# Optimization experiments

Measured on AMD Instinct MI355X. Metric: run time of the kernel, lower is better.

The kernel has to match this reference:

```python
import jax, jax.numpy as jnp
import numpy as np

N0, N1, N2 = 200000, 600000, 400000
NNZ1, NNZ2 = 1200000, 1200000
G = 256          # number of graphs in the batch
H = 128          # num_hidden
NIN = 32         # num_input
L = 2            # num_layers
R = 3            # max_rank + 1


def setup_inputs() -> dict:
    key = jax.random.key(0)
    ks = jax.random.split(key, 24)
    d = {}
    d["x0"] = jax.random.normal(ks[0], (N0, NIN), jnp.float32)
    d["x1"] = jax.random.normal(ks[1], (N1, NIN), jnp.float32)
    d["x2"] = jax.random.normal(ks[2], (N2, NIN), jnp.float32)
    d["b1_rows"] = jax.random.randint(ks[3], (NNZ1,), 0, N0, jnp.int32)
    d["b1_cols"] = jax.random.randint(ks[4], (NNZ1,), 0, N1, jnp.int32)
    d["b2_rows"] = jax.random.randint(ks[5], (NNZ2,), 0, N1, jnp.int32)
    d["b2_cols"] = jax.random.randint(ks[6], (NNZ2,), 0, N2, jnp.int32)
    d["batch0"] = jnp.sort(jax.random.randint(ks[7], (N0,), 0, G, jnp.int32))
    d["batch1"] = jnp.sort(jax.random.randint(ks[8], (N1,), 0, G, jnp.int32))
    d["batch2"] = jnp.sort(jax.random.randint(ks[9], (N2,), 0, G, jnp.int32))
    sin = 1.0 / np.sqrt(NIN).astype(np.float32)
    sh = 1.0 / np.sqrt(H).astype(np.float32)
    d["w_emb"] = jax.random.normal(ks[10], (NIN, H), jnp.float32) * sin
    d["b_emb"] = jnp.zeros((H,), jnp.float32)
    # one conv weight per (layer, rank>0): message W for B_r^T @ (x @ W)
    d["conv_w"] = jax.random.normal(ks[11], (L, 2, H, H), jnp.float32) * sh
    d["pre_w1"] = jax.random.normal(ks[12], (R, H, H), jnp.float32) * sh
    d["pre_b1"] = jnp.zeros((R, H), jnp.float32)
    d["pre_w2"] = jax.random.normal(ks[13], (R, H, H), jnp.float32) * sh
    d["pre_b2"] = jnp.zeros((R, H), jnp.float32)
    d["post_w1"] = jax.random.normal(ks[14], (R * H, H), jnp.float32) * (1.0 / np.sqrt(R * H).astype(np.float32))
    d["post_b1"] = jnp.zeros((H,), jnp.float32)
    d["post_w2"] = jax.random.normal(ks[15], (H, 1), jnp.float32) * sh
    d["post_b2"] = jnp.zeros((1,), jnp.float32)
    return d


def reference(x0, x1, x2, b1_rows, b1_cols, b2_rows, b2_cols,
              batch0, batch1, batch2,
              w_emb, b_emb, conv_w,
              pre_w1, pre_b1, pre_w2, pre_b2,
              post_w1, post_b1, post_w2, post_b2):
    # feature embedding (shared across ranks)
    h0 = x0 @ w_emb + b_emb
    h1 = x1 @ w_emb + b_emb
    h2 = x2 @ w_emb + b_emb

    for l in range(L):
        # sparse incidence matmul B_r^T @ h_{r-1}: gather rows, scatter-add to cols
        m1 = jax.ops.segment_sum(h0[b1_rows], b1_cols, num_segments=N1)
        m2 = jax.ops.segment_sum(h1[b2_rows], b2_cols, num_segments=N2)
        # aggregation with sigmoid update; rank 0 has no incoming messages
        h0 = jax.nn.sigmoid(h0)
        h1 = jax.nn.sigmoid(m1 @ conv_w[l, 0])
        h2 = jax.nn.sigmoid(m2 @ conv_w[l, 1])

    def pre_pool(h, r):
        z = jax.nn.silu(h @ pre_w1[r] + pre_b1[r])
        return z @ pre_w2[r] + pre_b2[r]

    # global_add_pool per rank -> [G, H] each
    p0 = jax.ops.segment_sum(pre_pool(h0, 0), batch0, num_segments=G)
    p1 = jax.ops.segment_sum(pre_pool(h1, 1), batch1, num_segments=G)
    p2 = jax.ops.segment_sum(pre_pool(h2, 2), batch2, num_segments=G)

    state = jnp.concatenate([p0, p1, p2], axis=1)  # [G, 3H]
    z = jax.nn.silu(state @ post_w1 + post_b1)
    out = z @ post_w2 + post_b2                     # [G, 1]
    return jnp.squeeze(out, axis=-1)                # [G]
```

## Files before the change

### kernel.cpp

```cpp
#include <hip/hip_runtime.h>
#include <math.h>

#define HDIM 128
#define NIN_ 32
#define RANKS 3

typedef unsigned int u32;
typedef unsigned short u16;
typedef __attribute__((ext_vector_type(8))) short short8;
typedef __attribute__((ext_vector_type(8))) __bf16 bf16x8;
typedef __attribute__((ext_vector_type(4))) float f32x4;

__device__ __forceinline__ float bf2f(u16 b) { return __uint_as_float(((u32)b) << 16); }
__device__ __forceinline__ u16 f2bf(float f) {
    u32 u = __float_as_uint(f);
    u32 r = u + 0x7fffu + ((u >> 16) & 1u);
    return (u16)(r >> 16);
}
__device__ __forceinline__ float sigmoidf_(float x) {
    return __builtin_amdgcn_rcpf(1.0f + __builtin_amdgcn_exp2f(-1.44269504f * x));
}
__device__ __forceinline__ float siluf_(float x) { return x * sigmoidf_(x); }

template <int SIG>
__device__ __forceinline__ float sigpow(float f) {
#pragma unroll
    for (int q = 0; q < SIG; ++q) f = sigmoidf_(f);
    return f;
}

__global__ void zero_kernel(u32* __restrict__ p, long long nw) {
    long long i = (long long)blockIdx.x * blockDim.x + threadIdx.x;
    long long stride = (long long)gridDim.x * blockDim.x;
    for (; i < nw; i += stride) p[i] = 0u;
}

__global__ void count_kernel(const int* __restrict__ cols, int* __restrict__ cnt, int nnz) {
    int e = blockIdx.x * 256 + threadIdx.x;
    if (e < nnz) atomicAdd(&cnt[cols[e]], 1);
}

__global__ void scan1_kernel(const int* __restrict__ cnt, int* __restrict__ bsum, int ndst) {
    __shared__ int lds[256];
    int base = blockIdx.x * 1024, t = threadIdx.x;
    int s = 0;
#pragma unroll
    for (int j = 0; j < 4; ++j) {
        int i = base + t * 4 + j;
        s += (i < ndst) ? cnt[i] : 0;
    }
    lds[t] = s;
    __syncthreads();
    for (int off = 128; off > 0; off >>= 1) {
        if (t < off) lds[t] += lds[t + off];
        __syncthreads();
    }
    if (t == 0) bsum[blockIdx.x] = lds[0];
}

__global__ void scan2_kernel(int* __restrict__ bsum, int nb, int* __restrict__ total) {
    __shared__ int lds[256];
    int t = threadIdx.x;
    int v[8];
    int s = 0;
#pragma unroll
    for (int j = 0; j < 8; ++j) {
        int i = t * 8 + j;
        v[j] = (i < nb) ? bsum[i] : 0;
        s += v[j];
    }
    lds[t] = s;
    __syncthreads();
    for (int off = 1; off < 256; off <<= 1) {
        int y = (t >= off) ? lds[t - off] : 0;
        __syncthreads();
        lds[t] += y;
        __syncthreads();
    }
    int run = lds[t] - s;
#pragma unroll
    for (int j = 0; j < 8; ++j) {
        int i = t * 8 + j;
        if (i < nb) {
            bsum[i] = run;
            run += v[j];
        }
    }
    if (t == 255) *total = run;
}

__global__ void scan3_kernel(const int* __restrict__ cnt, const int* __restrict__ bsum,
                             int* __restrict__ rowptr, int* __restrict__ cursor, int ndst) {
    __shared__ int lds[256];
    int base = blockIdx.x * 1024, t = threadIdx.x;
    int v[4];
    int s = 0;
#pragma unroll
    for (int j = 0; j < 4; ++j) {
        int i = base + t * 4 + j;
        v[j] = (i < ndst) ? cnt[i] : 0;
        s += v[j];
    }
    lds[t] = s;
    __syncthreads();
    for (int off = 1; off < 256; off <<= 1) {
        int y = (t >= off) ? lds[t - off] : 0;
        __syncthreads();
        lds[t] += y;
        __syncthreads();
    }
    int run = bsum[blockIdx.x] + lds[t] - s;
#pragma unroll
    for (int j = 0; j < 4; ++j) {
        int i = base + t * 4 + j;
        if (i < ndst) {
            rowptr[i] = run;
            cursor[i] = run;
            run += v[j];
        }
    }
}

__global__ void fill_kernel(const int* __restrict__ rows, const int* __restrict__ cols,
                            int* __restrict__ cursor, int* __restrict__ esrc, int nnz) {
    int e = blockIdx.x * 256 + threadIdx.x;
    if (e >= nnz) return;
    int idx = atomicAdd(&cursor[cols[e]], 1);
    esrc[idx] = rows[e];
}

__global__ void wprep_kernel(const float* __restrict__ conv_w, const float* __restrict__ pre_w1,
                             const float* __restrict__ pre_w2, u16* __restrict__ wt, int Lnum) {
    int tid = blockIdx.x * 256 + threadIdx.x;
    int nm = 2 * Lnum + 6;
    if (tid >= nm * 128 * 128) return;
    int m = tid >> 14;
    int r = tid & 16383;
    int k = r >> 7;
    int col = r & 127;
    const float* src;
    if (m < 2 * Lnum) src = conv_w + (size_t)m * 16384;
    else if (m < 2 * Lnum + 3) src = pre_w1 + (size_t)(m - 2 * Lnum) * 16384;
    else src = pre_w2 + (size_t)(m - 2 * Lnum - 3) * 16384;
    float v = src[k * 128 + col];
    wt[(size_t)m * 16384 + col * 128 + (k ^ ((col & 7) << 3))] = f2bf(v);
}

__global__ void wembprep_kernel(const float* __restrict__ w_emb, u16* __restrict__ wembT) {
    int tid = blockIdx.x * 256 + threadIdx.x;
    if (tid >= HDIM * NIN_) return;
    int col = tid >> 5, k = tid & 31;
    wembT[col * 32 + k] = f2bf(w_emb[k * HDIM + col]);
}

__global__ __launch_bounds__(512) void embed_mfma_kernel(const float* __restrict__ x,
                                                         const u16* __restrict__ wembT,
                                                         const float* __restrict__ b,
                                                         u16* __restrict__ h, int n) {
    __shared__ u16 cs[8][16][128];
    const int tid = threadIdx.x;
    const int wave = tid >> 6, lane = tid & 63;
    const int row0 = blockIdx.x * 128;
    const int col = lane & 15, kg = lane >> 4;
    const int wrow0 = row0 + wave * 16;
    const int arow = wrow0 + col;
    const int arowc = arow < n ? arow : (n - 1);

    bf16x8 afrag;
    {
        const float4* xp = (const float4*)(x + (size_t)arowc * NIN_ + kg * 8);
        float4 xa = xp[0], xb = xp[1];
        short8 s;
        s[0] = (short)f2bf(xa.x); s[1] = (short)f2bf(xa.y);
        s[2] = (short)f2bf(xa.z); s[3] = (short)f2bf(xa.w);
        s[4] = (short)f2bf(xb.x); s[5] = (short)f2bf(xb.y);
        s[6] = (short)f2bf(xb.z); s[7] = (short)f2bf(xb.w);
        afrag = __builtin_bit_cast(bf16x8, s);
    }

#pragma unroll
    for (int ct = 0; ct < 8; ++ct) {
        int bcol = ct * 16 + col;
        bf16x8 bfrag = *(const bf16x8*)(wembT + bcol * 32 + kg * 8);
        f32x4 acc = (f32x4){0.f, 0.f, 0.f, 0.f};
        acc = __builtin_amdgcn_mfma_f32_16x16x32_bf16(afrag, bfrag, acc, 0, 0, 0);
        float bv = b[bcol];
#pragma unroll
        for (int r = 0; r < 4; ++r) {
            int crow = kg * 4 + r;
            cs[wave][crow][(ct * 16 + col) ^ ((crow & 7) << 3)] = f2bf(acc[r] + bv);
        }
    }
#pragma unroll
    for (int it = 0; it < 4; ++it) {
        int cid = it * 64 + lane;
        int r = cid >> 4, c = cid & 15;
        int grow = wrow0 + r;
        if (grow < n) {
            short8 v = *(const short8*)(&cs[wave][r][(c * 8) ^ ((r & 7) << 3)]);
            *(short8*)(h + (size_t)grow * HDIM + c * 8) = v;
        }
    }
}

__device__ __forceinline__ void gemm128(const bf16x8 afrag[4], const u16* wls, f32x4 acc[8],
                                        int col, int kg) {
#pragma unroll
    for (int ct = 0; ct < 8; ++ct) {
        int bcol = ct * 16 + col;
        const u16* bb = wls + bcol * 128;
        int swz = (bcol & 7) << 3;
#pragma unroll
        for (int k0 = 0; k0 < 4; ++k0) {
            bf16x8 bfrag = *(const bf16x8*)(bb + ((k0 * 32 + kg * 8) ^ swz));
            acc[ct] = __builtin_amdgcn_mfma_f32_16x16x32_bf16(afrag[k0], bfrag, acc[ct], 0, 0, 0);
        }
    }
}

__device__ __forceinline__ void stage_w(const u16* __restrict__ w, u16* wls, int tid) {
    const uint4* g = (const uint4*)w;
    uint4* l = (uint4*)wls;
    for (int i = tid; i < 2048; i += 512) l[i] = g[i];
}

__device__ __forceinline__ void pool_acc(const f32x4 acc[8], const float* __restrict__ b2,
                                         const int* __restrict__ batch, float* __restrict__ p,
                                         int n, int colOff, int wrow0, int col, int kg) {
    if (wrow0 >= n) return;
    int rend = wrow0 + 15 < n ? wrow0 + 15 : (n - 1);
    int bstart = batch[wrow0];
    int bend = batch[rend];
    if (bstart == bend) {
#pragma unroll
        for (int ct = 0; ct < 8; ++ct) {
            float b2v = b2[ct * 16 + col];
            float s = 0.f;
#pragma unroll
            for (int r = 0; r < 4; ++r) {
                int row = wrow0 + kg * 4 + r;
                if (row < n) s += acc[ct][r] + b2v;
            }
            s += __shfl_xor(s, 16, 64);
            s += __shfl_xor(s, 32, 64);
            if (kg == 0) atomicAdd(&p[bstart * (RANKS * HDIM) + colOff + ct * 16 + col], s);
        }
    } else {
        int bgs[4];
#pragma unroll
        for (int r = 0; r < 4; ++r) {
            int row = wrow0 + kg * 4 + r;
            bgs[r] = (row < n) ? batch[row] : -1;
        }
#pragma unroll
        for (int ct = 0; ct < 8; ++ct) {
            float b2v = b2[ct * 16 + col];
            int curb = -1;
            float cur = 0.f;
#pragma unroll
            for (int r = 0; r < 4; ++r) {
                if (bgs[r] >= 0) {
                    if (bgs[r] != curb) {
                        if (curb >= 0)
                            atomicAdd(&p[curb * (RANKS * HDIM) + colOff + ct * 16 + col], cur);
                        curb = bgs[r];
                        cur = 0.f;
                    }
                    cur += acc[ct][r] + b2v;
                }
            }
            if (curb >= 0) atomicAdd(&p[curb * (RANKS * HDIM) + colOff + ct * 16 + col], cur);
        }
    }
}

template <int SIGA>
__global__ __launch_bounds__(512) void merged_n1_kernel(
    const u16* __restrict__ srcbuf, const int* __restrict__ rowptr,
    const int* __restrict__ esrc, const u16* __restrict__ wc0, const u16* __restrict__ wc1,
    const u16* __restrict__ w1t, const u16* __restrict__ w2t,
    const float* __restrict__ b1, const float* __restrict__ b2,
    const int* __restrict__ batch, float* __restrict__ p, int colOff,
    u16* __restrict__ outB, int n) {
    __shared__ u16 wls[16384];
    __shared__ u16 zs[8][16][128];
    const int tid = threadIdx.x;
    const int wave = tid >> 6, lane = tid & 63;
    const int row0 = blockIdx.x * 128;
    const int col = lane & 15, kg = lane >> 4;
    const int wrow0 = row0 + wave * 16;

    stage_w(wc0, wls, tid);

    float gr[4][8], gs[4][8];
#pragma unroll
    for (int k0 = 0; k0 < 4; ++k0)
#pragma unroll
        for (int j = 0; j < 8; ++j) { gr[k0][j] = 0.f; gs[k0][j] = 0.f; }

    const int arow = wrow0 + col;
    if (arow < n) {
        int beg = rowptr[arow], end = rowptr[arow + 1];
        for (int e = beg; e < end; e += 2) {
            int s0 = esrc[e];
            bool has1 = (e + 1 < end);
            int s1 = has1 ? esrc[e + 1] : s0;
            const bf16x8* p0 = (const bf16x8*)(srcbuf + (size_t)s0 * HDIM + kg * 8);
            const bf16x8* p1 = (const bf16x8*)(srcbuf + (size_t)s1 * HDIM + kg * 8);
            bf16x8 v0[4], v1[4];
#pragma unroll
            for (int k0 = 0; k0 < 4; ++k0) { v0[k0] = p0[k0 * 4]; v1[k0] = p1[k0 * 4]; }
#pragma unroll
            for (int k0 = 0; k0 < 4; ++k0) {
                short8 sv = __builtin_bit_cast(short8, v0[k0]);
#pragma unroll
                for (int j = 0; j < 8; ++j) {
                    float f = sigpow<SIGA>(bf2f((u16)sv[j]));
                    gr[k0][j] += f;
                    gs[k0][j] += sigmoidf_(f);
                }
            }
            if (has1) {
#pragma unroll
                for (int k0 = 0; k0 < 4; ++k0) {
                    short8 sv = __builtin_bit_cast(short8, v1[k0]);
#pragma unroll
                    for (int j = 0; j < 8; ++j) {
                        float f = sigpow<SIGA>(bf2f((u16)sv[j]));
                        gr[k0][j] += f;
                        gs[k0][j] += sigmoidf_(f);
                    }
                }
            }
        }
    }
    bf16x8 afragR[4], afragS[4];
#pragma unroll
    for (int k0 = 0; k0 < 4; ++k0) {
        short8 sR, sS;
#pragma unroll
        for (int j = 0; j < 8; ++j) {
            sR[j] = (short)f2bf(gr[k0][j]);
            sS[j] = (short)f2bf(gs[k0][j]);
        }
        afragR[k0] = __builtin_bit_cast(bf16x8, sR);
        afragS[k0] = __builtin_bit_cast(bf16x8, sS);
    }
    __syncthreads();

    f32x4 acc[8];
#pragma unroll
    for (int ct = 0; ct < 8; ++ct) acc[ct] = (f32x4){0.f, 0.f, 0.f, 0.f};
    gemm128(afragR, wls, acc, col, kg);
#pragma unroll
    for (int ct = 0; ct < 8; ++ct)
#pragma unroll
        for (int r = 0; r < 4; ++r) {
            int crow = kg * 4 + r;
            zs[wave][crow][(ct * 16 + col) ^ ((crow & 7) << 3)] = f2bf(sigmoidf_(acc[ct][r]));
        }
#pragma unroll
    for (int it = 0; it < 4; ++it) {
        int cid = it * 64 + lane;
        int r = cid >> 4, c = cid & 15;
        int grow = wrow0 + r;
        if (grow < n) {
            short8 v = *(const short8*)(&zs[wave][r][(c * 8) ^ ((r & 7) << 3)]);
            *(short8*)(outB + (size_t)grow * HDIM + c * 8) = v;
        }
    }

    __syncthreads();
    stage_w(wc1, wls, tid);
    __syncthreads();

#pragma unroll
    for (int ct = 0; ct < 8; ++ct) acc[ct] = (f32x4){0.f, 0.f, 0.f, 0.f};
    gemm128(afragS, wls, acc, col, kg);
#pragma unroll
    for (int ct = 0; ct < 8; ++ct)
#pragma unroll
        for (int r = 0; r < 4; ++r) {
            int crow = kg * 4 + r;
            zs[wave][crow][(ct * 16 + col) ^ ((crow & 7) << 3)] = f2bf(sigmoidf_(acc[ct][r]));
        }
    __syncthreads();
    stage_w(w1t, wls, tid);
    __syncthreads();

    bf16x8 zfrag[4];
    {
        int zswz = (col & 7) << 3;
#pragma unroll
        for (int k0 = 0; k0 < 4; ++k0)
            zfrag[k0] = *(const bf16x8*)(&zs[wave][col][(k0 * 32 + kg * 8) ^ zswz]);
    }
#pragma unroll
    for (int ct = 0; ct < 8; ++ct) acc[ct] = (f32x4){0.f, 0.f, 0.f, 0.f};
    gemm128(zfrag, wls, acc, col, kg);
#pragma unroll
    for (int ct = 0; ct < 8; ++ct) {
        float b1v = b1[ct * 16 + col];
#pragma unroll
        for (int r = 0; r < 4; ++r) {
            int crow = kg * 4 + r;
            zs[wave][crow][(ct * 16 + col) ^ ((crow & 7) << 3)] = f2bf(siluf_(acc[ct][r] + b1v));
        }
    }
    __syncthreads();
    stage_w(w2t, wls, tid);
    __syncthreads();

    {
        int zswz = (col & 7) << 3;
#pragma unroll
        for (int k0 = 0; k0 < 4; ++k0)
            zfrag[k0] = *(const bf16x8*)(&zs[wave][col][(k0 * 32 + kg * 8) ^ zswz]);
    }
#pragma unroll
    for (int ct = 0; ct < 8; ++ct) acc[ct] = (f32x4){0.f, 0.f, 0.f, 0.f};
    gemm128(zfrag, wls, acc, col, kg);

    pool_acc(acc, b2, batch, p, n, colOff, wrow0, col, kg);
}

template <int MODE, int SIG>
__global__ __launch_bounds__(512) void fused_mfma_kernel(
    const u16* __restrict__ srcbuf, const int* __restrict__ rowptr,
    const int* __restrict__ esrc, const u16* __restrict__ wconv,
    const u16* __restrict__ w1t, const u16* __restrict__ w2t,
    const float* __restrict__ b1, const float* __restrict__ b2,
    const int* __restrict__ batch, float* __restrict__ p, int colOff,
    u16* __restrict__ outB, int n) {
    __shared__ u16 wls[16384];
    __shared__ u16 zs[8][16][128];
    const int tid = threadIdx.x;
    const int wave = tid >> 6, lane = tid & 63;
    const int row0 = blockIdx.x * 128;
    const int col = lane & 15, kg = lane >> 4;
    const int wrow0 = row0 + wave * 16;

    stage_w(wconv, wls, tid);

    float ga[4][8];
#pragma unroll
    for (int k0 = 0; k0 < 4; ++k0)
#pragma unroll
        for (int j = 0; j < 8; ++j) ga[k0][j] = 0.f;
    const int arow = wrow0 + col;
    if (arow < n) {
        int beg = rowptr[arow], end = rowptr[arow + 1];
        for (int e = beg; e < end; e += 2) {
            int s0 = esrc[e];
            bool has1 = (e + 1 < end);
            int s1 = has1 ? esrc[e + 1] : s0;
            const bf16x8* p0 = (const bf16x8*)(srcbuf + (size_t)s0 * HDIM + kg * 8);
            const bf16x8* p1 = (const bf16x8*)(srcbuf + (size_t)s1 * HDIM + kg * 8);
            bf16x8 v0[4], v1[4];
#pragma unroll
            for (int k0 = 0; k0 < 4; ++k0) { v0[k0] = p0[k0 * 4]; v1[k0] = p1[k0 * 4]; }
#pragma unroll
            for (int k0 = 0; k0 < 4; ++k0) {
                short8 sv = __builtin_bit_cast(short8, v0[k0]);
#pragma unroll
                for (int j = 0; j < 8; ++j) ga[k0][j] += sigpow<SIG>(bf2f((u16)sv[j]));
            }
            if (has1) {
#pragma unroll
                for (int k0 = 0; k0 < 4; ++k0) {
                    short8 sv = __builtin_bit_cast(short8, v1[k0]);
#pragma unroll
                    for (int j = 0; j < 8; ++j) ga[k0][j] += sigpow<SIG>(bf2f((u16)sv[j]));
                }
            }
        }
    }
    bf16x8 afrag[4];
#pragma unroll
    for (int k0 = 0; k0 < 4; ++k0) {
        short8 s;
#pragma unroll
        for (int j = 0; j < 8; ++j) s[j] = (short)f2bf(ga[k0][j]);
        afrag[k0] = __builtin_bit_cast(bf16x8, s);
    }
    __syncthreads();

    f32x4 acc[8];
#pragma unroll
    for (int ct = 0; ct < 8; ++ct) acc[ct] = (f32x4){0.f, 0.f, 0.f, 0.f};
    gemm128(afrag, wls, acc, col, kg);

#pragma unroll
    for (int ct = 0; ct < 8; ++ct)
#pragma unroll
        for (int r = 0; r < 4; ++r) {
            int crow = kg * 4 + r;
            zs[wave][crow][(ct * 16 + col) ^ ((crow & 7) << 3)] = f2bf(sigmoidf_(acc[ct][r]));
        }

    if (MODE == 0) {
#pragma unroll
        for (int it = 0; it < 4; ++it) {
            int cid = it * 64 + lane;
            int r = cid >> 4, c = cid & 15;
            int grow = wrow0 + r;
            if (grow < n) {
                short8 v = *(const short8*)(&zs[wave][r][(c * 8) ^ ((r & 7) << 3)]);
                *(short8*)(outB + (size_t)grow * HDIM + c * 8) = v;
            }
        }
        return;
    }

    __syncthreads();
    stage_w(w1t, wls, tid);
    __syncthreads();

    bf16x8 zfrag[4];
    {
        int zswz = (col & 7) << 3;
#pragma unroll
        for (int k0 = 0; k0 < 4; ++k0)
            zfrag[k0] = *(const bf16x8*)(&zs[wave][col][(k0 * 32 + kg * 8) ^ zswz]);
    }
#pragma unroll
    for (int ct = 0; ct < 8; ++ct) acc[ct] = (f32x4){0.f, 0.f, 0.f, 0.f};
    gemm128(zfrag, wls, acc, col, kg);
#pragma unroll
    for (int ct = 0; ct < 8; ++ct) {
        float b1v = b1[ct * 16 + col];
#pragma unroll
        for (int r = 0; r < 4; ++r) {
            int crow = kg * 4 + r;
            zs[wave][crow][(ct * 16 + col) ^ ((crow & 7) << 3)] = f2bf(siluf_(acc[ct][r] + b1v));
        }
    }
    __syncthreads();
    stage_w(w2t, wls, tid);
    __syncthreads();

    {
        int zswz = (col & 7) << 3;
#pragma unroll
        for (int k0 = 0; k0 < 4; ++k0)
            zfrag[k0] = *(const bf16x8*)(&zs[wave][col][(k0 * 32 + kg * 8) ^ zswz]);
    }
#pragma unroll
    for (int ct = 0; ct < 8; ++ct) acc[ct] = (f32x4){0.f, 0.f, 0.f, 0.f};
    gemm128(zfrag, wls, acc, col, kg);

    pool_acc(acc, b2, batch, p, n, colOff, wrow0, col, kg);
}

template <int SIG>
__global__ __launch_bounds__(512) void prepool_mfma_kernel(
    const u16* __restrict__ h, const u16* __restrict__ w1t, const u16* __restrict__ w2t,
    const float* __restrict__ b1, const float* __restrict__ b2, const int* __restrict__ batch,
    float* __restrict__ p, int n, int colOff) {
    __shared__ u16 wls[16384];
    __shared__ u16 zs[8][16][128];
    const int tid = threadIdx.x;
    const int wave = tid >> 6, lane = tid & 63;
    const int row0 = blockIdx.x * 128;
    const int col = lane & 15, kg = lane >> 4;
    const int wrow0 = row0 + wave * 16;

    stage_w(w1t, wls, tid);

    const int arow = wrow0 + col;
    const int arowc = arow < n ? arow : (n - 1);
    bf16x8 afrag[4];
    {
        const bf16x8* ap = (const bf16x8*)(h + (size_t)arowc * HDIM + kg * 8);
#pragma unroll
        for (int k0 = 0; k0 < 4; ++k0) afrag[k0] = ap[k0 * 4];
    }
    if (SIG > 0) {
#pragma unroll
        for (int k0 = 0; k0 < 4; ++k0) {
            short8 s = __builtin_bit_cast(short8, afrag[k0]);
#pragma unroll
            for (int j = 0; j < 8; ++j) s[j] = (short)f2bf(sigpow<SIG>(bf2f((u16)s[j])));
            afrag[k0] = __builtin_bit_cast(bf16x8, s);
        }
    }
    __syncthreads();

    f32x4 acc[8];
#pragma unroll
    for (int ct = 0; ct < 8; ++ct) acc[ct] = (f32x4){0.f, 0.f, 0.f, 0.f};
    gemm128(afrag, wls, acc, col, kg);
#pragma unroll
    for (int ct = 0; ct < 8; ++ct) {
        float b1v = b1[ct * 16 + col];
#pragma unroll
        for (int r = 0; r < 4; ++r) {
            int crow = kg * 4 + r;
            zs[wave][crow][(ct * 16 + col) ^ ((crow & 7) << 3)] = f2bf(siluf_(acc[ct][r] + b1v));
        }
    }
    __syncthreads();
    stage_w(w2t, wls, tid);
    __syncthreads();

    bf16x8 zfrag[4];
    {
        int zswz = (col & 7) << 3;
#pragma unroll
        for (int k0 = 0; k0 < 4; ++k0)
            zfrag[k0] = *(const bf16x8*)(&zs[wave][col][(k0 * 32 + kg * 8) ^ zswz]);
    }
#pragma unroll
    for (int ct = 0; ct < 8; ++ct) acc[ct] = (f32x4){0.f, 0.f, 0.f, 0.f};
    gemm128(zfrag, wls, acc, col, kg);

    pool_acc(acc, b2, batch, p, n, colOff, wrow0, col, kg);
}

__global__ void final_kernel(const float* __restrict__ p, const float* __restrict__ w1,
                             const float* __restrict__ b1, const float* __restrict__ w2,
                             const float* __restrict__ b2, float* __restrict__ out) {
    const int g = blockIdx.x;
    const int c = threadIdx.x;
    const float* pg = p + g * (RANKS * HDIM);
    float acc = b1[c];
    for (int k = 0; k < RANKS * HDIM; ++k) acc = fmaf(pg[k], w1[k * HDIM + c], acc);
    float z = siluf_(acc);
    float v = z * w2[c];
#pragma unroll
    for (int off = 32; off > 0; off >>= 1) v += __shfl_down(v, off, 64);
    __shared__ float red[2];
    if ((c & 63) == 0) red[c >> 6] = v;
    __syncthreads();
    if (c == 0) out[g] = red[0] + red[1] + b2[0];
}

extern "C" void kernel_launch(void* const* d_in, const int* in_sizes, int n_in,
                              void* d_out, int out_size, void* d_ws, size_t ws_size,
                              hipStream_t stream) {
    const float* x0 = (const float*)d_in[0];
    const float* x1 = (const float*)d_in[1];
    const int* b1_rows = (const int*)d_in[3];
    const int* b1_cols = (const int*)d_in[4];
    const int* b2_rows = (const int*)d_in[5];
    const int* b2_cols = (const int*)d_in[6];
    const int* batch0 = (const int*)d_in[7];
    const int* batch1 = (const int*)d_in[8];
    const int* batch2 = (const int*)d_in[9];
    const float* w_emb = (const float*)d_in[10];
    const float* b_emb = (const float*)d_in[11];
    const float* conv_w = (const float*)d_in[12];
    const float* pre_w1 = (const float*)d_in[13];
    const float* pre_b1 = (const float*)d_in[14];
    const float* pre_w2 = (const float*)d_in[15];
    const float* pre_b2 = (const float*)d_in[16];
    const float* post_w1 = (const float*)d_in[17];
    const float* post_b1 = (const float*)d_in[18];
    const float* post_w2 = (const float*)d_in[19];
    const float* post_b2 = (const float*)d_in[20];

    const int N0 = in_sizes[0] / NIN_;
    const int N1 = in_sizes[1] / NIN_;
    const int N2 = in_sizes[2] / NIN_;
    const int NNZ1 = in_sizes[3];
    const int NNZ2 = in_sizes[5];
    const int L = in_sizes[12] / (2 * HDIM * HDIM);
    const int Gn = out_size;

    u16* A = (u16*)d_ws;
    u16* B = A + (size_t)N0 * HDIM;
    float* p = (float*)(B + (size_t)N1 * HDIM);
    u16* wt = (u16*)(p + (size_t)Gn * RANKS * HDIM);
    const u16* wt_conv = wt;
    const u16* wt_p1 = wt + (size_t)2 * L * 16384;
    const u16* wt_p2 = wt_p1 + (size_t)3 * 16384;
    u16* wembT = wt + (size_t)(2 * L + 6) * 16384;
    int* ip = (int*)(wembT + 4096);
    int* rowptr1 = ip;  ip += N1 + 1;
    int* rowptr2 = ip;  ip += N2 + 1;
    int* esrc1 = ip;    ip += NNZ1;
    int* esrc2 = ip;    ip += NNZ2;
    int maxN = N1 > N2 ? N1 : N2;
    int* cnt = ip;      ip += maxN;
    int* cursor = ip;   ip += maxN;
    int* bsum = ip;     ip += 2048;

    {
        int tot = (2 * L + 6) * 16384;
        wprep_kernel<<<(tot + 255) / 256, 256, 0, stream>>>(conv_w, pre_w1, pre_w2, wt, L);
        wembprep_kernel<<<16, 256, 0, stream>>>(w_emb, wembT);

        zero_kernel<<<512, 256, 0, stream>>>((u32*)cnt, N1);
        count_kernel<<<(NNZ1 + 255) / 256, 256, 0, stream>>>(b1_cols, cnt, NNZ1);
        int nb1 = (N1 + 1023) / 1024;
        scan1_kernel<<<nb1, 256, 0, stream>>>(cnt, bsum, N1);
        scan2_kernel<<<1, 256, 0, stream>>>(bsum, nb1, rowptr1 + N1);
        scan3_kernel<<<nb1, 256, 0, stream>>>(cnt, bsum, rowptr1, cursor, N1);
        fill_kernel<<<(NNZ1 + 255) / 256, 256, 0, stream>>>(b1_rows, b1_cols, cursor, esrc1, NNZ1);

        zero_kernel<<<512, 256, 0, stream>>>((u32*)cnt, N2);
        count_kernel<<<(NNZ2 + 255) / 256, 256, 0, stream>>>(b2_cols, cnt, NNZ2);
        int nb2 = (N2 + 1023) / 1024;
        scan1_kernel<<<nb2, 256, 0, stream>>>(cnt, bsum, N2);
        scan2_kernel<<<1, 256, 0, stream>>>(bsum, nb2, rowptr2 + N2);
        scan3_kernel<<<nb2, 256, 0, stream>>>(cnt, bsum, rowptr2, cursor, N2);
        fill_kernel<<<(NNZ2 + 255) / 256, 256, 0, stream>>>(b2_rows, b2_cols, cursor, esrc2, NNZ2);
    }

    embed_mfma_kernel<<<(N0 + 127) / 128, 512, 0, stream>>>(x0, wembT, b_emb, A, N0);

    zero_kernel<<<64, 256, 0, stream>>>((u32*)p, (long long)Gn * RANKS * HDIM);

    if (L >= 2) {
        int grid = (N1 + 127) / 128;
        const u16* wc0 = wt_conv + (size_t)((L - 2) * 2 + 0) * 16384;
        const u16* wc1 = wt_conv + (size_t)((L - 1) * 2 + 0) * 16384;
        switch (L - 2) {
            case 0: merged_n1_kernel<0><<<grid, 512, 0, stream>>>(
                        A, rowptr1, esrc1, wc0, wc1, wt_p1 + 16384, wt_p2 + 16384,
                        pre_b1 + HDIM, pre_b2 + HDIM, batch1, p, HDIM, B, N1); break;
            case 1: merged_n1_kernel<1><<<grid, 512, 0, stream>>>(
                        A, rowptr1, esrc1, wc0, wc1, wt_p1 + 16384, wt_p2 + 16384,
                        pre_b1 + HDIM, pre_b2 + HDIM, batch1, p, HDIM, B, N1); break;
            default: merged_n1_kernel<2><<<grid, 512, 0, stream>>>(
                        A, rowptr1, esrc1, wc0, wc1, wt_p1 + 16384, wt_p2 + 16384,
                        pre_b1 + HDIM, pre_b2 + HDIM, batch1, p, HDIM, B, N1); break;
        }
    } else {
        embed_mfma_kernel<<<(N1 + 127) / 128, 512, 0, stream>>>(x1, wembT, b_emb, B, N1);
        fused_mfma_kernel<1, 0><<<(N1 + 127) / 128, 512, 0, stream>>>(
            A, rowptr1, esrc1, wt_conv, wt_p1 + 16384, wt_p2 + 16384,
            pre_b1 + HDIM, pre_b2 + HDIM, batch1, p, HDIM, nullptr, N1);
    }

    fused_mfma_kernel<1, 0><<<(N2 + 127) / 128, 512, 0, stream>>>(
        B, rowptr2, esrc2, wt_conv + (size_t)((L - 1) * 2 + 1) * 16384,
        wt_p1 + 2 * 16384, wt_p2 + 2 * 16384, pre_b1 + 2 * HDIM, pre_b2 + 2 * HDIM,
        batch2, p, 2 * HDIM, nullptr, N2);

    {
        int grid = (N0 + 127) / 128;
        switch (L) {
            case 1: prepool_mfma_kernel<1><<<grid, 512, 0, stream>>>(
                        A, wt_p1, wt_p2, pre_b1, pre_b2, batch0, p, N0, 0); break;
            case 2: prepool_mfma_kernel<2><<<grid, 512, 0, stream>>>(
                        A, wt_p1, wt_p2, pre_b1, pre_b2, batch0, p, N0, 0); break;
            default: prepool_mfma_kernel<3><<<grid, 512, 0, stream>>>(
                        A, wt_p1, wt_p2, pre_b1, pre_b2, batch0, p, N0, 0); break;
        }
    }

    final_kernel<<<Gn, HDIM, 0, stream>>>(p, post_w1, post_b1, post_w2, post_b2, (float*)d_out);
}
```

Before: 794.1 us.

## Merge CSR build kernels for both incidences and prefetch next weight tile into registers

Builds both CSR structures together: one zero pass, one combined count kernel and one combined fill kernel, with separate count and cursor arrays, so there are fewer launches and more parallelism per launch. In the fused GEMM kernels, the next weight matrix is loaded into registers while the current stage computes, then written to LDS after the barrier, hiding global-load latency behind compute. It also swaps the manual bf16 conversion for the compiler's built-in cast. The register prefetch adds 16 VGPRs per thread and could lower occupancy; the larger workspace layout needs more memory.

```diff
diff --git a/kernel.cpp b/kernel.cpp
--- a/kernel.cpp
+++ b/kernel.cpp
@@ -11,12 +11,9 @@
 typedef __attribute__((ext_vector_type(8))) __bf16 bf16x8;
 typedef __attribute__((ext_vector_type(4))) float f32x4;
 
-__device__ __forceinline__ float bf2f(u16 b) { return __uint_as_float(((u32)b) << 16); }
-__device__ __forceinline__ u16 f2bf(float f) {
-    u32 u = __float_as_uint(f);
-    u32 r = u + 0x7fffu + ((u >> 16) & 1u);
-    return (u16)(r >> 16);
-}
+__device__ __forceinline__ u16 f2bf(float f) { return __builtin_bit_cast(u16, (__bf16)f); }
+__device__ __forceinline__ float bf2f(u16 b) { return (float)__builtin_bit_cast(__bf16, b); }
+
 __device__ __forceinline__ float sigmoidf_(float x) {
     return __builtin_amdgcn_rcpf(1.0f + __builtin_amdgcn_exp2f(-1.44269504f * x));
 }
@@ -35,9 +32,26 @@
     for (; i < nw; i += stride) p[i] = 0u;
 }
 
-__global__ void count_kernel(const int* __restrict__ cols, int* __restrict__ cnt, int nnz) {
+__global__ void count2_kernel(const int* __restrict__ c1, int n1, int* __restrict__ cntA,
+                              const int* __restrict__ c2, int n2, int* __restrict__ cntB) {
     int e = blockIdx.x * 256 + threadIdx.x;
-    if (e < nnz) atomicAdd(&cnt[cols[e]], 1);
+    if (e < n1) atomicAdd(&cntA[c1[e]], 1);
+    else if (e < n1 + n2) atomicAdd(&cntB[c2[e - n1]], 1);
+}
+
+__global__ void fill2_kernel(const int* __restrict__ r1, const int* __restrict__ c1,
+                             int* __restrict__ curA, int* __restrict__ esrc1, int n1,
+                             const int* __restrict__ r2, const int* __restrict__ c2,
+                             int* __restrict__ curB, int* __restrict__ esrc2, int n2) {
+    int e = blockIdx.x * 256 + threadIdx.x;
+    if (e < n1) {
+        int i = atomicAdd(&curA[c1[e]], 1);
+        esrc1[i] = r1[e];
+    } else if (e < n1 + n2) {
+        int ee = e - n1;
+        int i = atomicAdd(&curB[c2[ee]], 1);
+        esrc2[i] = r2[ee];
+    }
 }
 
 __global__ void scan1_kernel(const int* __restrict__ cnt, int* __restrict__ bsum, int ndst) {
@@ -119,14 +133,6 @@
             run += v[j];
         }
     }
-}
-
-__global__ void fill_kernel(const int* __restrict__ rows, const int* __restrict__ cols,
-                            int* __restrict__ cursor, int* __restrict__ esrc, int nnz) {
-    int e = blockIdx.x * 256 + threadIdx.x;
-    if (e >= nnz) return;
-    int idx = atomicAdd(&cursor[cols[e]], 1);
-    esrc[idx] = rows[e];
 }
 
 __global__ void wprep_kernel(const float* __restrict__ conv_w, const float* __restrict__ pre_w1,
@@ -221,7 +227,20 @@
 __device__ __forceinline__ void stage_w(const u16* __restrict__ w, u16* wls, int tid) {
     const uint4* g = (const uint4*)w;
     uint4* l = (uint4*)wls;
-    for (int i = tid; i < 2048; i += 512) l[i] = g[i];
+#pragma unroll
+    for (int i = 0; i < 4; ++i) l[tid + i * 512] = g[tid + i * 512];
+}
+
+__device__ __forceinline__ void prefetch_w(const u16* __restrict__ w, uint4 pw[4], int tid) {
+    const uint4* g = (const uint4*)w;
+#pragma unroll
+    for (int i = 0; i < 4; ++i) pw[i] = g[tid + i * 512];
+}
+
+__device__ __forceinline__ void commit_w(const uint4 pw[4], u16* wls, int tid) {
+    uint4* l = (uint4*)wls;
+#pragma unroll
+    for (int i = 0; i < 4; ++i) l[tid + i * 512] = pw[i];
 }
 
 __device__ __forceinline__ void pool_acc(const f32x4 acc[8], const float* __restrict__ b2,
@@ -291,6 +310,8 @@
     const int wrow0 = row0 + wave * 16;
 
     stage_w(wc0, wls, tid);
+    uint4 pw[4];
+    prefetch_w(wc1, pw, tid);
 
     float gr[4][8], gs[4][8];
 #pragma unroll
@@ -371,7 +392,8 @@
     }
 
     __syncthreads();
-    stage_w(wc1, wls, tid);
+    commit_w(pw, wls, tid);
+    prefetch_w(w1t, pw, tid);
     __syncthreads();
 
 #pragma unroll
@@ -385,7 +407,8 @@
             zs[wave][crow][(ct * 16 + col) ^ ((crow & 7) << 3)] = f2bf(sigmoidf_(acc[ct][r]));
         }
     __syncthreads();
-    stage_w(w1t, wls, tid);
+    commit_w(pw, wls, tid);
+    prefetch_w(w2t, pw, tid);
     __syncthreads();
 
     bf16x8 zfrag[4];
@@ -408,7 +431,7 @@
         }
     }
     __syncthreads();
-    stage_w(w2t, wls, tid);
+    commit_w(pw, wls, tid);
     __syncthreads();
 
     {
@@ -441,6 +464,8 @@
     const int wrow0 = row0 + wave * 16;
 
     stage_w(wconv, wls, tid);
+    uint4 pw[4];
+    if (MODE == 1) prefetch_w(w1t, pw, tid);
 
     float ga[4][8];
 #pragma unroll
@@ -513,7 +538,8 @@
     }
 
     __syncthreads();
-    stage_w(w1t, wls, tid);
+    commit_w(pw, wls, tid);
+    prefetch_w(w2t, pw, tid);
     __syncthreads();
 
     bf16x8 zfrag[4];
@@ -536,7 +562,7 @@
         }
     }
     __syncthreads();
-    stage_w(w2t, wls, tid);
+    commit_w(pw, wls, tid);
     __syncthreads();
 
     {
@@ -566,6 +592,8 @@
     const int wrow0 = row0 + wave * 16;
 
     stage_w(w1t, wls, tid);
+    uint4 pw[4];
+    prefetch_w(w2t, pw, tid);
 
     const int arow = wrow0 + col;
     const int arowc = arow < n ? arow : (n - 1);
@@ -600,7 +628,7 @@
         }
     }
     __syncthreads();
-    stage_w(w2t, wls, tid);
+    commit_w(pw, wls, tid);
     __syncthreads();
 
     bf16x8 zfrag[4];
@@ -680,9 +708,10 @@
     int* rowptr2 = ip;  ip += N2 + 1;
     int* esrc1 = ip;    ip += NNZ1;
     int* esrc2 = ip;    ip += NNZ2;
-    int maxN = N1 > N2 ? N1 : N2;
-    int* cnt = ip;      ip += maxN;
-    int* cursor = ip;   ip += maxN;
+    int* cntA = ip;     ip += N1;
+    int* cntB = ip;     ip += N2;
+    int* curA = ip;     ip += N1;
+    int* curB = ip;     ip += N2;
     int* bsum = ip;     ip += 2048;
 
     {
@@ -690,21 +719,19 @@
         wprep_kernel<<<(tot + 255) / 256, 256, 0, stream>>>(conv_w, pre_w1, pre_w2, wt, L);
         wembprep_kernel<<<16, 256, 0, stream>>>(w_emb, wembT);
 
-        zero_kernel<<<512, 256, 0, stream>>>((u32*)cnt, N1);
-        count_kernel<<<(NNZ1 + 255) / 256, 256, 0, stream>>>(b1_cols, cnt, NNZ1);
+        zero_kernel<<<1024, 256, 0, stream>>>((u32*)cntA, (long long)(N1 + N2));
+        count2_kernel<<<(NNZ1 + NNZ2 + 255) / 256, 256, 0, stream>>>(b1_cols, NNZ1, cntA,
+                                                                     b2_cols, NNZ2, cntB);
         int nb1 = (N1 + 1023) / 1024;
-        scan1_kernel<<<nb1, 256, 0, stream>>>(cnt, bsum, N1);
+        scan1_kernel<<<nb1, 256, 0, stream>>>(cntA, bsum, N1);
         scan2_kernel<<<1, 256, 0, stream>>>(bsum, nb1, rowptr1 + N1);
-        scan3_kernel<<<nb1, 256, 0, stream>>>(cnt, bsum, rowptr1, cursor, N1);
-        fill_kernel<<<(NNZ1 + 255) / 256, 256, 0, stream>>>(b1_rows, b1_cols, cursor, esrc1, NNZ1);
-
-        zero_kernel<<<512, 256, 0, stream>>>((u32*)cnt, N2);
-        count_kernel<<<(NNZ2 + 255) / 256, 256, 0, stream>>>(b2_cols, cnt, NNZ2);
+        scan3_kernel<<<nb1, 256, 0, stream>>>(cntA, bsum, rowptr1, curA, N1);
         int nb2 = (N2 + 1023) / 1024;
-        scan1_kernel<<<nb2, 256, 0, stream>>>(cnt, bsum, N2);
+        scan1_kernel<<<nb2, 256, 0, stream>>>(cntB, bsum, N2);
         scan2_kernel<<<1, 256, 0, stream>>>(bsum, nb2, rowptr2 + N2);
-        scan3_kernel<<<nb2, 256, 0, stream>>>(cnt, bsum, rowptr2, cursor, N2);
-        fill_kernel<<<(NNZ2 + 255) / 256, 256, 0, stream>>>(b2_rows, b2_cols, cursor, esrc2, NNZ2);
+        scan3_kernel<<<nb2, 256, 0, stream>>>(cntB, bsum, rowptr2, curB, N2);
+        fill2_kernel<<<(NNZ1 + NNZ2 + 255) / 256, 256, 0, stream>>>(
+            b1_rows, b1_cols, curA, esrc1, NNZ1, b2_rows, b2_cols, curB, esrc2, NNZ2);
     }
 
     embed_mfma_kernel<<<(N0 + 127) / 128, 512, 0, stream>>>(x0, wembT, b_emb, A, N0);
```

Measured after the change: 905.0 us. 14.0% more time.
